# Kernel tuning notes

Hardware: AMD Instinct MI355X
Metric: run time of the kernel (lower is better)

The kernel has to match this reference:

```python
import jax, jax.numpy as jnp
import numpy as np

N_NODES = 50000
N_EDGES = 800000
IN_CH = 64
OUT_CH = 64
PRIOR_VAR = 1.0


def setup_inputs() -> dict:
    key = jax.random.key(0)
    ks = jax.random.split(key, 10)
    mean = jax.random.normal(ks[0], (N_NODES, IN_CH), dtype=jnp.float32)
    std = jax.random.uniform(ks[1], (N_NODES, IN_CH), dtype=jnp.float32)
    edge_index = jax.random.randint(ks[2], (2, N_EDGES), 0, N_NODES, dtype=jnp.int32)
    edge_weight = jax.random.uniform(ks[3], (N_EDGES,), dtype=jnp.float32)
    # Bayesian GCN parameters (xavier-ish mu, log_sigma init -3.0) for mean- and std-branches
    scale = float(np.sqrt(6.0 / (IN_CH + OUT_CH)))
    mu_mean = jax.random.uniform(ks[4], (IN_CH, OUT_CH), minval=-scale, maxval=scale, dtype=jnp.float32)
    log_sigma_mean = jnp.full((IN_CH, OUT_CH), -3.0, dtype=jnp.float32)
    mu_std = jax.random.uniform(ks[5], (IN_CH, OUT_CH), minval=-scale, maxval=scale, dtype=jnp.float32)
    log_sigma_std = jnp.full((IN_CH, OUT_CH), -3.0, dtype=jnp.float32)
    # reparameterization noise (drawn once so reference is deterministic)
    eps_mean = jax.random.normal(ks[6], (IN_CH, OUT_CH), dtype=jnp.float32)
    eps_std = jax.random.normal(ks[7], (IN_CH, OUT_CH), dtype=jnp.float32)
    return {
        "mean": mean, "std": std, "edge_index": edge_index, "edge_weight": edge_weight,
        "mu_mean": mu_mean, "log_sigma_mean": log_sigma_mean, "eps_mean": eps_mean,
        "mu_std": mu_std, "log_sigma_std": log_sigma_std, "eps_std": eps_std,
    }


def _gcn_propagate(x, weight, edge_index, edge_weight):
    # support = x @ W; then gather src rows, scale by edge_weight, scatter-add to dst
    support = jnp.matmul(x, weight)                      # [N, out]
    src, dst = edge_index[0], edge_index[1]
    msg = edge_weight[:, None] * support[src]            # [E, out]
    return jax.ops.segment_sum(msg, dst, num_segments=N_NODES)


def _kl(mu, log_sigma):
    pv = PRIOR_VAR
    kl = 0.5 * (jnp.exp(2.0 * log_sigma) / pv + mu ** 2 / pv
                - 2.0 * log_sigma - jnp.log(jnp.asarray(pv, mu.dtype)) - 1.0)
    return kl.sum()


def reference(mean, std, edge_index, edge_weight,
              mu_mean, log_sigma_mean, eps_mean,
              mu_std, log_sigma_std, eps_std):
    # mean branch
    w_mean = mu_mean + eps_mean * jnp.exp(log_sigma_mean)
    new_mean = _gcn_propagate(mean, w_mean, edge_index, edge_weight)
    kl_mean = _kl(mu_mean, log_sigma_mean)
    # std branch operates on variance with squared edge weights
    var = std ** 2
    w_std = mu_std + eps_std * jnp.exp(log_sigma_std)
    new_log_var = _gcn_propagate(var, w_std, edge_index, edge_weight ** 2)
    kl_std = _kl(mu_std, log_sigma_std)
    new_std = jnp.sqrt(jnp.exp(new_log_var) + 1e-6)
    total_kl = kl_mean + kl_std
    return (new_mean, new_std, total_kl)
```

## Files before the change

kernel.cpp:

```cpp
#include <hip/hip_runtime.h>

#define N_NODES 50000
#define N_EDGES 800000
#define CH 64
#define OUT_OFF_STD (N_NODES * CH)
#define OUT_OFF_KL  (2 * N_NODES * CH)
#define CAP 64
#define CAP_USE 62

#define NGRP 8
#define NPG 6250
#define FILL_CHUNK 2048
#define FILL_CHUNKS 391
#define FILL_BLOCKS (NGRP * FILL_CHUNKS)
#define GEMM_BLOCKS 782
#define GATHER_CHUNKS 1563
#define ZERO_GRID 208

typedef __attribute__((ext_vector_type(8))) short short8;
typedef __attribute__((ext_vector_type(4))) float f32x4;

__device__ __forceinline__ int rl_i(unsigned v, int lane) {
    return __builtin_amdgcn_readlane((int)v, lane);
}
__device__ __forceinline__ unsigned f2bf(float f) {
    unsigned u = __float_as_uint(f);
    return (u + 0x7fffu + ((u >> 16) & 1u)) >> 16;
}
__device__ __forceinline__ int* cnt_ptr(uint2* bins, int node) {
    return (int*)(bins + (size_t)node * CAP + 63);
}

__global__ __launch_bounds__(256) void wkl_kernel(
    const float* __restrict__ mu_m, const float* __restrict__ ls_m,
    const float* __restrict__ eps_m,
    const float* __restrict__ mu_s, const float* __restrict__ ls_s,
    const float* __restrict__ eps_s,
    unsigned short* __restrict__ fragBm, unsigned short* __restrict__ fragBv,
    float* __restrict__ kl_out, uint2* __restrict__ bins)
{
    if (blockIdx.x != 0) {
        if (blockIdx.x < 8) return;
        const int g = blockIdx.x & (NGRP - 1);
        const int loc = ((int)(blockIdx.x >> 3) - 1) * 256 + (int)threadIdx.x;
        if (loc < NPG) *cnt_ptr(bins, g * NPG + loc) = 0;
        return;
    }
    __shared__ unsigned short Wm[CH * CH];
    __shared__ unsigned short Wv[CH * CH];
    float kl = 0.0f;
    for (int i = threadIdx.x; i < CH * CH; i += 256) {
        float mu = mu_m[i], ls = ls_m[i];
        Wm[i] = (unsigned short)f2bf(mu + eps_m[i] * expf(ls));
        kl += 0.5f * (expf(2.0f * ls) + mu * mu - 2.0f * ls - 1.0f);
        mu = mu_s[i]; ls = ls_s[i];
        Wv[i] = (unsigned short)f2bf(mu + eps_s[i] * expf(ls));
        kl += 0.5f * (expf(2.0f * ls) + mu * mu - 2.0f * ls - 1.0f);
    }
    __syncthreads();
    for (int f = threadIdx.x; f < CH * CH; f += 256) {
        int j = f & 7, l = (f >> 3) & 63, ch = f >> 9;
        int k = (ch & 1) * 32 + ((l >> 4) & 3) * 8 + j;
        int n = (ch >> 1) * 16 + (l & 15);
        fragBm[f] = Wm[k * CH + n];
        fragBv[f] = Wv[k * CH + n];
    }
    for (int off = 32; off > 0; off >>= 1)
        kl += __shfl_down(kl, off, 64);
    __shared__ float red[4];
    if ((threadIdx.x & 63) == 0) red[threadIdx.x >> 6] = kl;
    __syncthreads();
    if (threadIdx.x == 0)
        kl_out[0] = red[0] + red[1] + red[2] + red[3];
}

__global__ __launch_bounds__(256) void gemfill_kernel(
    const float* __restrict__ mean, const float* __restrict__ stdv,
    const unsigned short* __restrict__ fragBm,
    const unsigned short* __restrict__ fragBv,
    const int* __restrict__ ei, const float* __restrict__ ew,
    uint2* __restrict__ bins, unsigned* __restrict__ sup)
{
    const int tid = threadIdx.x;

    if (blockIdx.x < FILL_BLOCKS) {
        const int g = blockIdx.x & (NGRP - 1);
        const int chunk = blockIdx.x >> 3;
        const int base = chunk * FILL_CHUNK + tid * 8;
        const int lo = g * NPG;

        int d[8], s[8]; float w[8];
        if (base + 8 <= N_EDGES) {
            int4 d0 = *(const int4*)(ei + N_EDGES + base);
            int4 d1 = *(const int4*)(ei + N_EDGES + base + 4);
            d[0] = d0.x; d[1] = d0.y; d[2] = d0.z; d[3] = d0.w;
            d[4] = d1.x; d[5] = d1.y; d[6] = d1.z; d[7] = d1.w;
            int4 s0 = *(const int4*)(ei + base);
            int4 s1 = *(const int4*)(ei + base + 4);
            s[0] = s0.x; s[1] = s0.y; s[2] = s0.z; s[3] = s0.w;
            s[4] = s1.x; s[5] = s1.y; s[6] = s1.z; s[7] = s1.w;
            float4 w0 = *(const float4*)(ew + base);
            float4 w1 = *(const float4*)(ew + base + 4);
            w[0] = w0.x; w[1] = w0.y; w[2] = w0.z; w[3] = w0.w;
            w[4] = w1.x; w[5] = w1.y; w[6] = w1.z; w[7] = w1.w;
        } else {
#pragma unroll
            for (int t = 0; t < 8; ++t) {
                bool v = (base + t) < N_EDGES;
                d[t] = v ? ei[N_EDGES + base + t] : -1;
                s[t] = v ? ei[base + t] : 0;
                w[t] = v ? ew[base + t] : 0.0f;
            }
        }

        int slot[8];
#pragma unroll
        for (int t = 0; t < 8; ++t) {
            bool act = (unsigned)(d[t] - lo) < (unsigned)NPG;
            slot[t] = act ? atomicAdd(cnt_ptr(bins, d[t]), 1) : CAP;
        }
#pragma unroll
        for (int t = 0; t < 8; ++t) {
            if (slot[t] < CAP_USE)
                bins[(size_t)d[t] * CAP + slot[t]] =
                    make_uint2((unsigned)s[t], __float_as_uint(w[t]));
        }
        return;
    }

    const int lane = tid & 63, wave = tid >> 6;
    const int row0 = (blockIdx.x - FILL_BLOCKS) * 64 + wave * 16;
    if (row0 >= N_NODES) return;

    const int m = lane & 15;
    const int q = (lane >> 4) & 3;
    const float* mrow = mean + (size_t)(row0 + m) * CH + q * 8;
    const float* srow = stdv + (size_t)(row0 + m) * CH + q * 8;

    short8 aM[2], aV[2];
#pragma unroll
    for (int h = 0; h < 2; ++h) {
        float4 x0 = *(const float4*)(mrow + h * 32);
        float4 x1 = *(const float4*)(mrow + h * 32 + 4);
        float4 s0 = *(const float4*)(srow + h * 32);
        float4 s1 = *(const float4*)(srow + h * 32 + 4);
        aM[h][0] = (short)f2bf(x0.x); aM[h][1] = (short)f2bf(x0.y);
        aM[h][2] = (short)f2bf(x0.z); aM[h][3] = (short)f2bf(x0.w);
        aM[h][4] = (short)f2bf(x1.x); aM[h][5] = (short)f2bf(x1.y);
        aM[h][6] = (short)f2bf(x1.z); aM[h][7] = (short)f2bf(x1.w);
        aV[h][0] = (short)f2bf(s0.x * s0.x); aV[h][1] = (short)f2bf(s0.y * s0.y);
        aV[h][2] = (short)f2bf(s0.z * s0.z); aV[h][3] = (short)f2bf(s0.w * s0.w);
        aV[h][4] = (short)f2bf(s1.x * s1.x); aV[h][5] = (short)f2bf(s1.y * s1.y);
        aV[h][6] = (short)f2bf(s1.z * s1.z); aV[h][7] = (short)f2bf(s1.w * s1.w);
    }

    f32x4 accM[4], accV[4];
#pragma unroll
    for (int c = 0; c < 4; ++c) {
        accM[c] = (f32x4)0.0f;
        accV[c] = (f32x4)0.0f;
    }
#pragma unroll
    for (int c = 0; c < 4; ++c) {
#pragma unroll
        for (int h = 0; h < 2; ++h) {
            short8 bm = *(const short8*)(fragBm + ((c * 2 + h) * 64 + lane) * 8);
            short8 bv = *(const short8*)(fragBv + ((c * 2 + h) * 64 + lane) * 8);
            accM[c] = __builtin_amdgcn_mfma_f32_16x16x32_bf16(aM[h], bm, accM[c], 0, 0, 0);
            accV[c] = __builtin_amdgcn_mfma_f32_16x16x32_bf16(aV[h], bv, accV[c], 0, 0, 0);
        }
    }

    const int rg = lane >> 4;
#pragma unroll
    for (int c = 0; c < 4; ++c) {
#pragma unroll
        for (int r = 0; r < 4; ++r) {
            int node = row0 + rg * 4 + r;
            sup[(size_t)node * CH + c * 16 + m] =
                f2bf(accM[c][r]) | (f2bf(accV[c][r]) << 16);
        }
    }
}

__global__ __launch_bounds__(256) void gather_kernel(
    const uint2* __restrict__ bins,
    const unsigned* __restrict__ sup, float* __restrict__ out)
{
    const int g = blockIdx.x & (NGRP - 1);
    const int cid = blockIdx.x >> 3;
    const int wave = threadIdx.x >> 6;
    const int col = threadIdx.x & 63;
    const int loc = cid * 4 + wave;
    if (loc >= NPG) return;
    const int n = g * NPG + loc;

    int cnt = *(const int*)(bins + (size_t)n * CAP + 63);
    if (cnt > CAP_USE) cnt = CAP_USE;
    uint2 p = make_uint2(0u, 0u);
    if (col < cnt) p = bins[(size_t)n * CAP + col];

    float accM = 0.0f, accV = 0.0f;
    for (int i = 0; i < cnt; i += 8) {
        int   s[8];
        float w[8];
#pragma unroll
        for (int t = 0; t < 8; ++t) {
            bool v = (i + t < cnt);
            s[t] = v ? rl_i(p.x, i + t) : 0;
            w[t] = v ? __uint_as_float((unsigned)rl_i(p.y, i + t)) : 0.0f;
        }
        unsigned q[8];
#pragma unroll
        for (int t = 0; t < 8; ++t)
            q[t] = sup[(size_t)s[t] * CH + col];
#pragma unroll
        for (int t = 0; t < 8; ++t) {
            float mm = __uint_as_float(q[t] << 16);
            float vv = __uint_as_float(q[t] & 0xFFFF0000u);
            accM += w[t] * mm;
            accV += (w[t] * w[t]) * vv;
        }
    }
    out[(size_t)n * CH + col] = accM;
    out[OUT_OFF_STD + (size_t)n * CH + col] = sqrtf(expf(accV) + 1e-6f);
}

extern "C" void kernel_launch(void* const* d_in, const int* in_sizes, int n_in,
                              void* d_out, int out_size, void* d_ws, size_t ws_size,
                              hipStream_t stream)
{
    const float* mean  = (const float*)d_in[0];
    const float* stdv  = (const float*)d_in[1];
    const int*   ei    = (const int*)d_in[2];
    const float* ew    = (const float*)d_in[3];
    const float* mu_m  = (const float*)d_in[4];
    const float* ls_m  = (const float*)d_in[5];
    const float* eps_m = (const float*)d_in[6];
    const float* ls_s  = (const float*)d_in[8];
    const float* mu_s  = (const float*)d_in[7];
    const float* eps_s = (const float*)d_in[9];

    float* out = (float*)d_out;
    unsigned*       sup    = (unsigned*)d_ws;
    uint2*          bins   = (uint2*)(sup + (size_t)N_NODES * CH);
    unsigned short* fragBm = (unsigned short*)(bins + (size_t)N_NODES * CAP);
    unsigned short* fragBv = fragBm + CH * CH;

    wkl_kernel<<<ZERO_GRID, 256, 0, stream>>>(
        mu_m, ls_m, eps_m, mu_s, ls_s, eps_s,
        fragBm, fragBv, out + OUT_OFF_KL, bins);
    gemfill_kernel<<<FILL_BLOCKS + GEMM_BLOCKS, 256, 0, stream>>>(
        mean, stdv, fragBm, fragBv, ei, ew, bins, sup);
    gather_kernel<<<NGRP * GATHER_CHUNKS, 256, 0, stream>>>(bins, sup, out);
}
```

Baseline: 176.3 us.

## Persistent gather waves with bin prefetch and deeper unrolled loads

Turns the gather kernel into a grid-stride persistent kernel in which each wave handles several nodes. It prefetches the next node's bin row while working on the current one, reads the count from the bin row through a lane read instead of a separate load, issues 24 independent row loads up front, and writes outputs with nontemporal stores. The fill kernel now processes 16 edges per thread instead of 8, halving the block count. These changes aim to hide gather latency and cut launch and scheduling overhead, at the cost of more registers and redundant loads for nodes with few edges.

```diff
diff --git a/kernel.cpp b/kernel.cpp
--- a/kernel.cpp
+++ b/kernel.cpp
@@ -10,11 +10,12 @@
 
 #define NGRP 8
 #define NPG 6250
-#define FILL_CHUNK 2048
-#define FILL_CHUNKS 391
+#define FILL_CHUNK 4096
+#define FILL_CHUNKS 196
 #define FILL_BLOCKS (NGRP * FILL_CHUNKS)
 #define GEMM_BLOCKS 782
-#define GATHER_CHUNKS 1563
+#define GATHER_BLOCKS 2048
+#define GWAVES_PG 1024
 #define ZERO_GRID 208
 
 typedef __attribute__((ext_vector_type(8))) short short8;
@@ -86,26 +87,32 @@
     if (blockIdx.x < FILL_BLOCKS) {
         const int g = blockIdx.x & (NGRP - 1);
         const int chunk = blockIdx.x >> 3;
-        const int base = chunk * FILL_CHUNK + tid * 8;
+        const int base = chunk * FILL_CHUNK + tid * 16;
         const int lo = g * NPG;
 
-        int d[8], s[8]; float w[8];
-        if (base + 8 <= N_EDGES) {
-            int4 d0 = *(const int4*)(ei + N_EDGES + base);
-            int4 d1 = *(const int4*)(ei + N_EDGES + base + 4);
-            d[0] = d0.x; d[1] = d0.y; d[2] = d0.z; d[3] = d0.w;
-            d[4] = d1.x; d[5] = d1.y; d[6] = d1.z; d[7] = d1.w;
-            int4 s0 = *(const int4*)(ei + base);
-            int4 s1 = *(const int4*)(ei + base + 4);
-            s[0] = s0.x; s[1] = s0.y; s[2] = s0.z; s[3] = s0.w;
-            s[4] = s1.x; s[5] = s1.y; s[6] = s1.z; s[7] = s1.w;
-            float4 w0 = *(const float4*)(ew + base);
-            float4 w1 = *(const float4*)(ew + base + 4);
-            w[0] = w0.x; w[1] = w0.y; w[2] = w0.z; w[3] = w0.w;
-            w[4] = w1.x; w[5] = w1.y; w[6] = w1.z; w[7] = w1.w;
+        int d[16], s[16]; float w[16];
+        if (base + 16 <= N_EDGES) {
+#pragma unroll
+            for (int h = 0; h < 4; ++h) {
+                int4 dv = *(const int4*)(ei + N_EDGES + base + h * 4);
+                d[h * 4 + 0] = dv.x; d[h * 4 + 1] = dv.y;
+                d[h * 4 + 2] = dv.z; d[h * 4 + 3] = dv.w;
+            }
+#pragma unroll
+            for (int h = 0; h < 4; ++h) {
+                int4 sv = *(const int4*)(ei + base + h * 4);
+                s[h * 4 + 0] = sv.x; s[h * 4 + 1] = sv.y;
+                s[h * 4 + 2] = sv.z; s[h * 4 + 3] = sv.w;
+            }
+#pragma unroll
+            for (int h = 0; h < 4; ++h) {
+                float4 wv = *(const float4*)(ew + base + h * 4);
+                w[h * 4 + 0] = wv.x; w[h * 4 + 1] = wv.y;
+                w[h * 4 + 2] = wv.z; w[h * 4 + 3] = wv.w;
+            }
         } else {
 #pragma unroll
-            for (int t = 0; t < 8; ++t) {
+            for (int t = 0; t < 16; ++t) {
                 bool v = (base + t) < N_EDGES;
                 d[t] = v ? ei[N_EDGES + base + t] : -1;
                 s[t] = v ? ei[base + t] : 0;
@@ -113,14 +120,14 @@
             }
         }
 
-        int slot[8];
-#pragma unroll
-        for (int t = 0; t < 8; ++t) {
+        int slot[16];
+#pragma unroll
+        for (int t = 0; t < 16; ++t) {
             bool act = (unsigned)(d[t] - lo) < (unsigned)NPG;
             slot[t] = act ? atomicAdd(cnt_ptr(bins, d[t]), 1) : CAP;
         }
 #pragma unroll
-        for (int t = 0; t < 8; ++t) {
+        for (int t = 0; t < 16; ++t) {
             if (slot[t] < CAP_USE)
                 bins[(size_t)d[t] * CAP + slot[t]] =
                     make_uint2((unsigned)s[t], __float_as_uint(w[t]));
@@ -188,42 +195,62 @@
     const unsigned* __restrict__ sup, float* __restrict__ out)
 {
     const int g = blockIdx.x & (NGRP - 1);
-    const int cid = blockIdx.x >> 3;
-    const int wave = threadIdx.x >> 6;
+    const int wid = ((int)(blockIdx.x >> 3)) * 4 + (int)(threadIdx.x >> 6);
     const int col = threadIdx.x & 63;
-    const int loc = cid * 4 + wave;
+    const int nbase = g * NPG;
+
+    int loc = wid;
     if (loc >= NPG) return;
-    const int n = g * NPG + loc;
-
-    int cnt = *(const int*)(bins + (size_t)n * CAP + 63);
-    if (cnt > CAP_USE) cnt = CAP_USE;
-    uint2 p = make_uint2(0u, 0u);
-    if (col < cnt) p = bins[(size_t)n * CAP + col];
-
-    float accM = 0.0f, accV = 0.0f;
-    for (int i = 0; i < cnt; i += 8) {
-        int   s[8];
-        float w[8];
-#pragma unroll
-        for (int t = 0; t < 8; ++t) {
-            bool v = (i + t < cnt);
-            s[t] = v ? rl_i(p.x, i + t) : 0;
-            w[t] = v ? __uint_as_float((unsigned)rl_i(p.y, i + t)) : 0.0f;
-        }
-        unsigned q[8];
-#pragma unroll
-        for (int t = 0; t < 8; ++t)
-            q[t] = sup[(size_t)s[t] * CH + col];
-#pragma unroll
-        for (int t = 0; t < 8; ++t) {
-            float mm = __uint_as_float(q[t] << 16);
-            float vv = __uint_as_float(q[t] & 0xFFFF0000u);
-            accM += w[t] * mm;
-            accV += (w[t] * w[t]) * vv;
-        }
-    }
-    out[(size_t)n * CH + col] = accM;
-    out[OUT_OFF_STD + (size_t)n * CH + col] = sqrtf(expf(accV) + 1e-6f);
+
+    uint2 pnext = bins[(size_t)(nbase + loc) * CAP + col];
+
+    for (; loc < NPG; loc += GWAVES_PG) {
+        uint2 p = pnext;
+        {
+            int loc2 = loc + GWAVES_PG;
+            if (loc2 < NPG)
+                pnext = bins[(size_t)(nbase + loc2) * CAP + col];
+        }
+        int cnt = rl_i(p.x, 63);
+        if (cnt > CAP_USE) cnt = CAP_USE;
+
+        float accM = 0.0f, accV = 0.0f;
+        if (cnt > 0) {
+            unsigned q[24];
+#pragma unroll
+            for (int t = 0; t < 24; ++t) {
+                int e = (t < cnt) ? t : (cnt - 1);
+                q[t] = sup[(size_t)(unsigned)rl_i(p.x, e) * CH + col];
+            }
+#pragma unroll
+            for (int t = 0; t < 24; ++t) {
+                int e = (t < cnt) ? t : (cnt - 1);
+                float wt = (t < cnt)
+                    ? __uint_as_float((unsigned)rl_i(p.y, e)) : 0.0f;
+                accM += wt * __uint_as_float(q[t] << 16);
+                accV += (wt * wt) * __uint_as_float(q[t] & 0xFFFF0000u);
+            }
+            for (int i = 24; i < cnt; i += 8) {
+                unsigned qq[8]; float ww[8];
+#pragma unroll
+                for (int t = 0; t < 8; ++t) {
+                    int e = (i + t < cnt) ? (i + t) : (cnt - 1);
+                    qq[t] = sup[(size_t)(unsigned)rl_i(p.x, e) * CH + col];
+                    ww[t] = (i + t < cnt)
+                        ? __uint_as_float((unsigned)rl_i(p.y, e)) : 0.0f;
+                }
+#pragma unroll
+                for (int t = 0; t < 8; ++t) {
+                    accM += ww[t] * __uint_as_float(qq[t] << 16);
+                    accV += (ww[t] * ww[t]) * __uint_as_float(qq[t] & 0xFFFF0000u);
+                }
+            }
+        }
+        const int n = nbase + loc;
+        __builtin_nontemporal_store(accM, &out[(size_t)n * CH + col]);
+        __builtin_nontemporal_store(sqrtf(expf(accV) + 1e-6f),
+                                    &out[OUT_OFF_STD + (size_t)n * CH + col]);
+    }
 }
 
 extern "C" void kernel_launch(void* const* d_in, const int* in_sizes, int n_in,
@@ -252,5 +279,5 @@
         fragBm, fragBv, out + OUT_OFF_KL, bins);
     gemfill_kernel<<<FILL_BLOCKS + GEMM_BLOCKS, 256, 0, stream>>>(
         mean, stdv, fragBm, fragBv, ei, ew, bins, sup);
-    gather_kernel<<<NGRP * GATHER_CHUNKS, 256, 0, stream>>>(bins, sup, out);
-}
+    gather_kernel<<<GATHER_BLOCKS, 256, 0, stream>>>(bins, sup, out);
+}
```

Result: no change. 174.4 us (-1.1%).
